# Kernel tuning notes

Measured on AMD Instinct MI355X. Metric: run time of the kernel, lower is better.

## Reference

```python
import jax, jax.numpy as jnp
import numpy as np

# dims
Z, P, N, H = 16, 4, 466, 86          # z_dim, p_dim, n_dim, gmean(466,16)
B_SZ, T = 2048, 32                   # batch, number of eval times
INNER = 16                           # fixed trial-step budget per eval interval
ATOL, RTOL = 1e-20, 1e-5
H2B, H3B = 64, 2048                  # B-net hiddens: int(sqrt(16**3)), 16**3//2

# Dormand-Prince 5(4) tableau
A21 = 1/5
A31, A32 = 3/40, 9/40
A41, A42, A43 = 44/45, -56/15, 32/9
A51, A52, A53, A54 = 19372/6561, -25360/2187, 64448/6561, -212/729
A61, A62, A63, A64, A65 = 9017/3168, -355/33, 46732/5247, 49/176, -5103/18656
B1, B3, B4, B5, B6 = 35/384, 500/1113, 125/192, -2187/6784, 11/84
E1, E3, E4, E5, E6, E7 = 71/57600, -71/16695, 71/1920, -17253/339200, 22/525, -1/40


def _leaky(x):
    return jnp.where(x >= 0, x, 0.2 * x)


def setup_inputs() -> dict:
    key = jax.random.key(0)
    ks = jax.random.split(key, 26)
    w = lambda k, shape: (jax.random.normal(k, shape) * 0.05).astype(jnp.float32)
    inp = {}
    inp['n_0'] = jax.random.normal(ks[0], (B_SZ, N), dtype=jnp.float32)
    inp['p'] = jax.random.uniform(ks[1], (P,), dtype=jnp.float32)
    inp['tstep'] = jnp.arange(T, dtype=jnp.float32) / (T - 1)
    # autoencoder
    inp['We1'], inp['be1'] = w(ks[2], (N, H)), w(ks[3], (H,))
    inp['We2'], inp['be2'] = w(ks[4], (H, Z)), w(ks[5], (Z,))
    inp['Wd1'], inp['bd1'] = w(ks[6], (Z, H)), w(ks[7], (H,))
    inp['Wd2'], inp['bd2'] = w(ks[8], (H, N)), w(ks[9], (N,))
    # A net: P -> Z -> Z*Z//2 -> Z*Z
    inp['Wa1'], inp['ba1'] = w(ks[10], (P, Z)), w(ks[11], (Z,))
    inp['Wa2'], inp['ba2'] = w(ks[12], (Z, Z*Z//2)), w(ks[13], (Z*Z//2,))
    inp['Wa3'], inp['ba3'] = w(ks[14], (Z*Z//2, Z*Z)), w(ks[15], (Z*Z,))
    # B net: P -> Z -> 64 -> 2048 -> Z**3
    inp['Wb1'], inp['bb1'] = w(ks[16], (P, Z)), w(ks[17], (Z,))
    inp['Wb2'], inp['bb2'] = w(ks[18], (Z, H2B)), w(ks[19], (H2B,))
    inp['Wb3'], inp['bb3'] = w(ks[20], (H2B, H3B)), w(ks[21], (H3B,))
    inp['Wb4'], inp['bb4'] = w(ks[22], (H3B, Z**3)), w(ks[23], (Z**3,))
    return inp


def _solve(z0, tstep, Amat, Bten):
    # adaptive Dopri5 with integral (I) step-size controller; fixed trial budget per interval
    def f(z):  # g(z,p): A z + B z z
        return z @ Amat.T + jnp.einsum('ijk,bj,bk->bi', Bten, z, z)

    def step(y, dt):
        k1 = f(y)
        k2 = f(y + dt * (A21 * k1))
        k3 = f(y + dt * (A31 * k1 + A32 * k2))
        k4 = f(y + dt * (A41 * k1 + A42 * k2 + A43 * k3))
        k5 = f(y + dt * (A51 * k1 + A52 * k2 + A53 * k3 + A54 * k4))
        k6 = f(y + dt * (A61 * k1 + A62 * k2 + A63 * k3 + A64 * k4 + A65 * k5))
        y5 = y + dt * (B1 * k1 + B3 * k3 + B4 * k4 + B5 * k5 + B6 * k6)
        k7 = f(y5)
        err = dt * (E1 * k1 + E3 * k3 + E4 * k4 + E5 * k5 + E6 * k6 + E7 * k7)
        return y5, err

    def interval(carry, tpair):
        y, dt = carry
        t0, t1 = tpair[0], tpair[1]

        def inner(c, _):
            t, y, dt = c
            done = t >= t1 - 1e-10
            dtc = jnp.where(done, 0.0, jnp.minimum(dt, t1 - t))  # clip to interval end
            ynew, err = step(y, dtc)
            tol = ATOL + RTOL * jnp.maximum(jnp.abs(y), jnp.abs(ynew))
            en = jnp.sqrt(jnp.mean((err / tol) ** 2))
            accept = (en <= 1.0) & (~done)
            t = jnp.where(accept, t + dtc, t)
            y = jnp.where(accept, ynew, y)
            factor = jnp.clip(0.9 * jnp.maximum(en, 1e-12) ** -0.2, 0.2, 10.0)
            dt = jnp.where(done, dt, dt * factor)
            return (t, y, dt), None

        (tf, yf, dtf), _ = jax.lax.scan(inner, (t0, y, dt), None, length=INNER)
        return (yf, dtf), yf

    dt0 = (tstep[1] - tstep[0]) * 0.3
    tpairs = jnp.stack([tstep[:-1], tstep[1:]], axis=1)  # [T-1, 2]
    (_, _), ys = jax.lax.scan(interval, (z0, dt0), tpairs)
    return jnp.concatenate([z0[None], ys], axis=0)  # [T, b, Z]


def reference(n_0, p, tstep, We1, be1, We2, be2, Wd1, bd1, Wd2, bd2,
              Wa1, ba1, Wa2, ba2, Wa3, ba3,
              Wb1, bb1, Wb2, bb2, Wb3, bb3, Wb4, bb4):
    # encoder
    z0 = _leaky(n_0 @ We1 + be1) @ We2 + be2  # [b, Z]
    # A(p), B(p) depend only on p -> computed once per solve
    ha = _leaky(p @ Wa1 + ba1)
    ha = _leaky(ha @ Wa2 + ba2)
    Amat = _leaky(ha @ Wa3 + ba3).reshape(Z, Z)
    hb = _leaky(p @ Wb1 + bb1)
    hb = _leaky(hb @ Wb2 + bb2)
    hb = _leaky(hb @ Wb3 + bb3)
    Bten = _leaky(hb @ Wb4 + bb4).reshape(Z, Z, Z)
    zs = _solve(z0, tstep, Amat, Bten)  # [T, b, Z]
    # decoder
    return _leaky(zs @ Wd1 + bd1) @ Wd2 + bd2  # [T, b, N]
```

## Files before the change

### kernel.cpp

```cpp
#include <hip/hip_runtime.h>
#include <cmath>

#define DEV __device__ __forceinline__

static DEV float leakyf(float x){ return x >= 0.0f ? x : 0.2f*x; }

typedef float v2f __attribute__((ext_vector_type(2)));

constexpr float cA21 = (float)(1.0/5.0);
constexpr float cA31 = (float)(3.0/40.0),  cA32 = (float)(9.0/40.0);
constexpr float cA41 = (float)(44.0/45.0), cA42 = (float)(-56.0/15.0), cA43 = (float)(32.0/9.0);
constexpr float cA51 = (float)(19372.0/6561.0), cA52 = (float)(-25360.0/2187.0);
constexpr float cA53 = (float)(64448.0/6561.0), cA54 = (float)(-212.0/729.0);
constexpr float cA61 = (float)(9017.0/3168.0),  cA62 = (float)(-355.0/33.0);
constexpr float cA63 = (float)(46732.0/5247.0), cA64 = (float)(49.0/176.0);
constexpr float cA65 = (float)(-5103.0/18656.0);
constexpr float cB1 = (float)(35.0/384.0),  cB3 = (float)(500.0/1113.0), cB4 = (float)(125.0/192.0);
constexpr float cB5 = (float)(-2187.0/6784.0), cB6 = (float)(11.0/84.0);
constexpr float cE1 = (float)(71.0/57600.0), cE3 = (float)(-71.0/16695.0), cE4 = (float)(71.0/1920.0);
constexpr float cE5 = (float)(-17253.0/339200.0), cE6 = (float)(22.0/525.0), cE7 = (float)(-1.0/40.0);

#define WS_AMAT   0
#define WS_HB3    256
#define WS_BTEN   2304
#define WS_ZS     6400
#define WS_SLOTSF (6400 + 1048576)
#define WS_SB2    (WS_SLOTSF + 253952)

__global__ void __launch_bounds__(256) k_smallnets(
    const float* __restrict__ p,
    const float* __restrict__ Wa1, const float* __restrict__ ba1,
    const float* __restrict__ Wa2, const float* __restrict__ ba2,
    const float* __restrict__ Wa3, const float* __restrict__ ba3,
    const float* __restrict__ Wb1, const float* __restrict__ bb1,
    const float* __restrict__ Wb2, const float* __restrict__ bb2,
    float* __restrict__ wsf)
{
    __shared__ float sp[4], sa1[16], sa2[128], sb1[16];
    int tid = threadIdx.x;
    if (tid < 4) sp[tid] = p[tid];
    __syncthreads();
    if (tid < 16) {
        float a = ba1[tid];
        for (int j = 0; j < 4; ++j) a = fmaf(sp[j], Wa1[j*16+tid], a);
        sa1[tid] = leakyf(a);
        float c = bb1[tid];
        for (int j = 0; j < 4; ++j) c = fmaf(sp[j], Wb1[j*16+tid], c);
        sb1[tid] = leakyf(c);
    }
    __syncthreads();
    if (tid < 128) {
        float a = ba2[tid];
        for (int j = 0; j < 16; ++j) a = fmaf(sa1[j], Wa2[j*128+tid], a);
        sa2[tid] = leakyf(a);
    }
    if (tid < 64) {
        float c = bb2[tid];
        for (int j = 0; j < 16; ++j) c = fmaf(sb1[j], Wb2[j*64+tid], c);
        wsf[WS_SB2 + tid] = leakyf(c);
    }
    __syncthreads();
    {
        float a = ba3[tid];
        for (int j = 0; j < 128; ++j) a = fmaf(sa2[j], Wa3[j*256+tid], a);
        wsf[WS_AMAT + tid] = leakyf(a);
    }
}

__global__ void __launch_bounds__(256) k_hb3(
    const float* __restrict__ Wb3, const float* __restrict__ bb3, float* __restrict__ wsf)
{
    __shared__ float sb2[64];
    int tid = threadIdx.x;
    if (tid < 64) sb2[tid] = wsf[WS_SB2 + tid];
    __syncthreads();
    int o = blockIdx.x * 256 + tid;
    float c = bb3[o];
    for (int j = 0; j < 64; ++j) c = fmaf(sb2[j], Wb3[(size_t)j*2048 + o], c);
    wsf[WS_HB3 + o] = leakyf(c);
}

__global__ void __launch_bounds__(256) k_bten(
    const float* __restrict__ Wb4, const float* __restrict__ bb4, float* __restrict__ wsf)
{
    __shared__ float red[256];
    const float* hb3 = wsf + WS_HB3;
    float* Bten = wsf + WS_BTEN;
    int tid = threadIdx.x;
    int ol = tid & 15, part = tid >> 4;
    int o = blockIdx.x * 16 + ol;
    float a = 0.0f;
    for (int q = 0; q < 128; ++q) {
        int hh = part*128 + q;
        a = fmaf(hb3[hh], Wb4[(size_t)hh*4096 + o], a);
    }
    red[part*16 + ol] = a;
    __syncthreads();
    for (int s = 8; s >= 1; s >>= 1) {
        if (part < s) red[part*16+ol] += red[(part+s)*16+ol];
        __syncthreads();
    }
    if (tid < 16) {
        float v = red[tid] + bb4[blockIdx.x*16 + tid];
        Bten[blockIdx.x*16 + tid] = leakyf(v);
    }
}

__global__ void __launch_bounds__(256) k_encoder(
    const float* __restrict__ n0,
    const float* __restrict__ We1, const float* __restrict__ be1,
    const float* __restrict__ We2, const float* __restrict__ be2,
    float* __restrict__ zs)
{
    __shared__ float hL[8][88];
    int tid = threadIdx.x;
    int r = tid >> 5, c = tid & 31;
    int row = blockIdx.x * 8 + r;
    const float* nrow = n0 + (size_t)row * 466;
    int c2 = (c + 64 < 86) ? (c + 64) : 85;
    float a0 = 0.f, a1 = 0.f, a2 = 0.f;
    for (int n = 0; n < 466; ++n) {
        float nv = nrow[n];
        a0 = fmaf(nv, We1[n*86 + c], a0);
        a1 = fmaf(nv, We1[n*86 + c + 32], a1);
        a2 = fmaf(nv, We1[n*86 + c2], a2);
    }
    hL[r][c]      = leakyf(a0 + be1[c]);
    hL[r][c + 32] = leakyf(a1 + be1[c + 32]);
    if (c < 22) hL[r][c + 64] = leakyf(a2 + be1[c + 64]);
    __syncthreads();
    if (tid < 128) {
        int r2 = tid >> 4, ii = tid & 15;
        int row2 = blockIdx.x * 8 + r2;
        float a = be2[ii];
        #pragma unroll
        for (int hh = 0; hh < 86; ++hh) a = fmaf(hL[r2][hh], We2[hh*16 + ii], a);
        zs[(size_t)row2 * 16 + ii] = a;
    }
}

__global__ void __launch_bounds__(256) k_solver(
    const float* __restrict__ tstep, float* __restrict__ wsf)
{
    __shared__ float zL[8][16];
    __shared__ float redA[2][4], redB[2][4];
    float* Amat = wsf + WS_AMAT;
    float* Bten = wsf + WS_BTEN;
    float* zs   = wsf + WS_ZS;
    unsigned long long* slots = (unsigned long long*)(wsf + WS_SLOTSF);

    const int tid = threadIdx.x, blk = blockIdx.x;
    const int e = tid >> 5, g = tid & 31;
    const int i = g >> 1, h = g & 1, h8 = h * 8;
    const int b = blk * 8 + e;

    v2f Bl2[64], aR2[8];
    #pragma unroll
    for (int p = 0; p < 8; ++p) {
        int jA = (h8 + 2*p)     & 15;
        int jB = (h8 + 2*p + 1) & 15;
        v2f ap; ap.x = (h == 0) ? Amat[i*16 + 2*p] : 0.0f;
        ap.y = (h == 0) ? Amat[i*16 + 2*p + 1] : 0.0f;
        aR2[p] = ap;
        const float4* bpA = (const float4*)(Bten + i*256 + jA*16 + h8);
        const float4* bpB = (const float4*)(Bten + i*256 + jB*16 + h8);
        float4 a0 = bpA[0], a1 = bpA[1], b0 = bpB[0], b1 = bpB[1];
        v2f q;
        q.x=a0.x; q.y=b0.x; Bl2[p*8+0]=q;  q.x=a0.y; q.y=b0.y; Bl2[p*8+1]=q;
        q.x=a0.z; q.y=b0.z; Bl2[p*8+2]=q;  q.x=a0.w; q.y=b0.w; Bl2[p*8+3]=q;
        q.x=a1.x; q.y=b1.x; Bl2[p*8+4]=q;  q.x=a1.y; q.y=b1.y; Bl2[p*8+5]=q;
        q.x=a1.z; q.y=b1.z; Bl2[p*8+6]=q;  q.x=a1.w; q.y=b1.w; Bl2[p*8+7]=q;
    }

    float y = zs[(size_t)b*16 + i];

    auto feval = [&](float zi) -> float {
        zL[e][i] = zi;
        const float4* zp = (const float4*)(&zL[e][0]);
        int q0 = h8 >> 2;
        float4 r0 = zp[q0], r1 = zp[(q0+1)&3], r2 = zp[(q0+2)&3], r3 = zp[(q0+3)&3];
        float zz[16] = { r0.x,r0.y,r0.z,r0.w, r1.x,r1.y,r1.z,r1.w,
                         r2.x,r2.y,r2.z,r2.w, r3.x,r3.y,r3.z,r3.w };
        v2f zb[8];
        #pragma unroll
        for (int kk = 0; kk < 8; ++kk) { v2f t; t.x = zz[kk]; t.y = zz[kk]; zb[kk] = t; }
        v2f t2[8];
        #pragma unroll
        for (int p = 0; p < 8; ++p) t2[p] = aR2[p];
        #pragma unroll
        for (int p = 0; p < 8; ++p) {
            #pragma unroll
            for (int kk = 0; kk < 8; ++kk)
                asm("v_pk_fma_f32 %0, %1, %2, %0" : "+v"(t2[p]) : "v"(Bl2[p*8+kk]), "v"(zb[kk]));
        }
        float acc = 0.0f;
        #pragma unroll
        for (int p = 0; p < 8; ++p) {
            acc = fmaf(zz[2*p],     t2[p].x, acc);
            acc = fmaf(zz[2*p + 1], t2[p].y, acc);
        }
        acc += __shfl_xor(acc, 1);
        return acc;
    };

    float dt = (tstep[1] - tstep[0]) * 0.3f;
    float k1 = feval(y), k2, k3, k4, k5, k6, k7;
    int stepIdx = 0;

    for (int iv = 0; iv < 31; ++iv) {
        float t  = tstep[iv];
        float t1 = tstep[iv + 1];
        for (int it = 0; it < 16; ++it) {
            if (t >= t1 - 1e-10f) break;
            float dtc = fminf(dt, t1 - t);

            float z2 = fmaf(dtc, cA21*k1, y);                                         k2 = feval(z2);
            float z3 = fmaf(dtc, fmaf(cA32,k2, cA31*k1), y);                          k3 = feval(z3);
            float z4 = fmaf(dtc, fmaf(cA43,k3, fmaf(cA42,k2, cA41*k1)), y);           k4 = feval(z4);
            float z5 = fmaf(dtc, fmaf(cA54,k4, fmaf(cA53,k3, fmaf(cA52,k2, cA51*k1))), y);
            k5 = feval(z5);
            float z6 = fmaf(dtc, fmaf(cA65,k5, fmaf(cA64,k4, fmaf(cA63,k3, fmaf(cA62,k2, cA61*k1)))), y);
            k6 = feval(z6);
            float y5 = fmaf(dtc, fmaf(cB6,k6, fmaf(cB5,k5, fmaf(cB4,k4, fmaf(cB3,k3, cB1*k1)))), y);
            k7 = feval(y5);
            float err = dtc * fmaf(cE7,k7, fmaf(cE6,k6, fmaf(cE5,k5, fmaf(cE4,k4, fmaf(cE3,k3, cE1*k1)))));

            float ay = fabsf(y), a5 = fabsf(y5);
            float mx = (ay > a5) ? ay : a5;
            float tol = fmaf(1e-5f, mx, 1e-20f);
            float r = err / tol;
            float r2 = r * r;

            const int par = stepIdx & 1;

            float w = r2;
            w += __shfl_xor(w, 1);  w += __shfl_xor(w, 2);  w += __shfl_xor(w, 4);
            w += __shfl_xor(w, 8);  w += __shfl_xor(w, 16); w += __shfl_xor(w, 32);
            if ((tid & 63) == 0) redA[par][tid >> 6] = w;
            __syncthreads();
            float bsum = ((redA[par][0] + redA[par][1]) + redA[par][2]) + redA[par][3];

            unsigned long long* rowp = slots + (size_t)stepIdx * 256;
            if (tid == 0) {
                unsigned long long pv = (1ull << 32) | (unsigned long long)__float_as_uint(bsum);
                __hip_atomic_store(&rowp[blk], pv, __ATOMIC_RELAXED, __HIP_MEMORY_SCOPE_AGENT);
            }
            unsigned long long v = __hip_atomic_load(&rowp[tid], __ATOMIC_RELAXED, __HIP_MEMORY_SCOPE_AGENT);
            if ((unsigned)(v >> 32) != 1u) {
                for (;;) {
                    unsigned long long va = __hip_atomic_load(&rowp[tid], __ATOMIC_RELAXED, __HIP_MEMORY_SCOPE_AGENT);
                    unsigned long long vb = __hip_atomic_load(&rowp[tid], __ATOMIC_RELAXED, __HIP_MEMORY_SCOPE_AGENT);
                    if ((unsigned)(va >> 32) == 1u) { v = va; break; }
                    if ((unsigned)(vb >> 32) == 1u) { v = vb; break; }
                }
            }
            float ps = __uint_as_float((unsigned)v);
            ps += __shfl_xor(ps, 1);  ps += __shfl_xor(ps, 2);  ps += __shfl_xor(ps, 4);
            ps += __shfl_xor(ps, 8);  ps += __shfl_xor(ps, 16); ps += __shfl_xor(ps, 32);
            if ((tid & 63) == 0) redB[par][tid >> 6] = ps;
            __syncthreads();
            float gsum = ((redB[par][0] + redB[par][1]) + redB[par][2]) + redB[par][3];
            ++stepIdx;

            float en = sqrtf(gsum * (1.0f / 65536.0f));

            if (!(en == en)) {
                if (h == 0) {
                    for (int s = iv + 1; s < 32; ++s)
                        zs[((size_t)s * 2048 + b) * 16 + i] = y;
                }
                return;
            }
            if (en <= 1.0f) { t = t + dtc; y = y5; k1 = k7; }
            float fac = 0.9f * powf(fmaxf(en, 1e-12f), -0.2f);
            fac = fminf(fmaxf(fac, 0.2f), 10.0f);
            dt = dt * fac;
        }
        if (h == 0) zs[((size_t)(iv + 1) * 2048 + b) * 16 + i] = y;
    }
}

__global__ void __launch_bounds__(256) k_decoder(
    const float* __restrict__ zs,
    const float* __restrict__ Wd1, const float* __restrict__ bd1,
    const float* __restrict__ Wd2, const float* __restrict__ bd2,
    float* __restrict__ out)
{
    __shared__ __align__(16) float hT[86][16];
    int tid = threadIdx.x;
    size_t rowbase = (size_t)blockIdx.x * 16;

    for (int v = tid; v < 86*16; v += 256) {
        int hh = v >> 4, r = v & 15;
        const float4* z4 = (const float4*)(zs + (rowbase + r) * 16);
        float4 za = z4[0], zb = z4[1], zc = z4[2], zd = z4[3];
        float a = bd1[hh];
        a = fmaf(za.x, Wd1[ 0*86 + hh], a);  a = fmaf(za.y, Wd1[ 1*86 + hh], a);
        a = fmaf(za.z, Wd1[ 2*86 + hh], a);  a = fmaf(za.w, Wd1[ 3*86 + hh], a);
        a = fmaf(zb.x, Wd1[ 4*86 + hh], a);  a = fmaf(zb.y, Wd1[ 5*86 + hh], a);
        a = fmaf(zb.z, Wd1[ 6*86 + hh], a);  a = fmaf(zb.w, Wd1[ 7*86 + hh], a);
        a = fmaf(zc.x, Wd1[ 8*86 + hh], a);  a = fmaf(zc.y, Wd1[ 9*86 + hh], a);
        a = fmaf(zc.z, Wd1[10*86 + hh], a);  a = fmaf(zc.w, Wd1[11*86 + hh], a);
        a = fmaf(zd.x, Wd1[12*86 + hh], a);  a = fmaf(zd.y, Wd1[13*86 + hh], a);
        a = fmaf(zd.z, Wd1[14*86 + hh], a);  a = fmaf(zd.w, Wd1[15*86 + hh], a);
        hT[hh][r] = leakyf(a);
    }
    __syncthreads();

    for (int c = tid; c < 466; c += 256) {
        float acc[16];
        #pragma unroll
        for (int r = 0; r < 16; ++r) acc[r] = bd2[c];
        for (int hh = 0; hh < 86; ++hh) {
            float w = Wd2[hh*466 + c];
            const float4* hp = (const float4*)(&hT[hh][0]);
            float4 h0 = hp[0], h1 = hp[1], h2 = hp[2], h3 = hp[3];
            acc[ 0] = fmaf(h0.x, w, acc[ 0]);  acc[ 1] = fmaf(h0.y, w, acc[ 1]);
            acc[ 2] = fmaf(h0.z, w, acc[ 2]);  acc[ 3] = fmaf(h0.w, w, acc[ 3]);
            acc[ 4] = fmaf(h1.x, w, acc[ 4]);  acc[ 5] = fmaf(h1.y, w, acc[ 5]);
            acc[ 6] = fmaf(h1.z, w, acc[ 6]);  acc[ 7] = fmaf(h1.w, w, acc[ 7]);
            acc[ 8] = fmaf(h2.x, w, acc[ 8]);  acc[ 9] = fmaf(h2.y, w, acc[ 9]);
            acc[10] = fmaf(h2.z, w, acc[10]);  acc[11] = fmaf(h2.w, w, acc[11]);
            acc[12] = fmaf(h3.x, w, acc[12]);  acc[13] = fmaf(h3.y, w, acc[13]);
            acc[14] = fmaf(h3.z, w, acc[14]);  acc[15] = fmaf(h3.w, w, acc[15]);
        }
        #pragma unroll
        for (int r = 0; r < 16; ++r) out[(rowbase + r) * 466 + c] = acc[r];
    }
}

extern "C" void kernel_launch(void* const* d_in, const int* in_sizes, int n_in,
                              void* d_out, int out_size, void* d_ws, size_t ws_size,
                              hipStream_t stream)
{
    const float* n0   = (const float*)d_in[0];
    const float* p    = (const float*)d_in[1];
    const float* tstep= (const float*)d_in[2];
    const float* We1  = (const float*)d_in[3];  const float* be1 = (const float*)d_in[4];
    const float* We2  = (const float*)d_in[5];  const float* be2 = (const float*)d_in[6];
    const float* Wd1  = (const float*)d_in[7];  const float* bd1 = (const float*)d_in[8];
    const float* Wd2  = (const float*)d_in[9];  const float* bd2 = (const float*)d_in[10];
    const float* Wa1  = (const float*)d_in[11]; const float* ba1 = (const float*)d_in[12];
    const float* Wa2  = (const float*)d_in[13]; const float* ba2 = (const float*)d_in[14];
    const float* Wa3  = (const float*)d_in[15]; const float* ba3 = (const float*)d_in[16];
    const float* Wb1  = (const float*)d_in[17]; const float* bb1 = (const float*)d_in[18];
    const float* Wb2  = (const float*)d_in[19]; const float* bb2 = (const float*)d_in[20];
    const float* Wb3  = (const float*)d_in[21]; const float* bb3 = (const float*)d_in[22];
    const float* Wb4  = (const float*)d_in[23]; const float* bb4 = (const float*)d_in[24];
    float* out = (float*)d_out;
    float* wsf = (float*)d_ws;

    hipLaunchKernelGGL(k_smallnets, dim3(1), dim3(256), 0, stream,
                       p, Wa1, ba1, Wa2, ba2, Wa3, ba3, Wb1, bb1, Wb2, bb2, wsf);
    hipLaunchKernelGGL(k_hb3, dim3(8), dim3(256), 0, stream, Wb3, bb3, wsf);
    hipLaunchKernelGGL(k_bten, dim3(256), dim3(256), 0, stream, Wb4, bb4, wsf);
    hipLaunchKernelGGL(k_encoder, dim3(256), dim3(256), 0, stream,
                       n0, We1, be1, We2, be2, wsf + WS_ZS);

    hipLaunchKernelGGL(k_solver, dim3(256), dim3(256), 0, stream, tstep, wsf);

    hipLaunchKernelGGL(k_decoder, dim3(4096), dim3(256), 0, stream,
                       wsf + WS_ZS, Wd1, bd1, Wd2, bd2, out);
}
```

Before: 1.349 ms.

## Fuse encoder into solver kernel and exchange state via ds_bpermute

Moves the encoder computation into the start of the solver kernel, so z0 is produced in shared memory and one kernel launch plus the global round-trip are removed. It also replaces the per-stage shared-memory write and float4 reads of the state vector inside feval with 16 ds_bpermute cross-lane reads, which removes LDS stores and the associated synchronisation-like dependency. The trade-off is more register pressure for the permutation indices and 16 bpermute instructions per evaluation instead of four vector LDS loads.

```diff
diff --git a/kernel.cpp b/kernel.cpp
--- a/kernel.cpp
+++ b/kernel.cpp
@@ -106,43 +106,15 @@
     }
 }
 
-__global__ void __launch_bounds__(256) k_encoder(
+__global__ void __launch_bounds__(256) k_solver(
+    const float* __restrict__ tstep,
     const float* __restrict__ n0,
     const float* __restrict__ We1, const float* __restrict__ be1,
     const float* __restrict__ We2, const float* __restrict__ be2,
-    float* __restrict__ zs)
-{
-    __shared__ float hL[8][88];
-    int tid = threadIdx.x;
-    int r = tid >> 5, c = tid & 31;
-    int row = blockIdx.x * 8 + r;
-    const float* nrow = n0 + (size_t)row * 466;
-    int c2 = (c + 64 < 86) ? (c + 64) : 85;
-    float a0 = 0.f, a1 = 0.f, a2 = 0.f;
-    for (int n = 0; n < 466; ++n) {
-        float nv = nrow[n];
-        a0 = fmaf(nv, We1[n*86 + c], a0);
-        a1 = fmaf(nv, We1[n*86 + c + 32], a1);
-        a2 = fmaf(nv, We1[n*86 + c2], a2);
-    }
-    hL[r][c]      = leakyf(a0 + be1[c]);
-    hL[r][c + 32] = leakyf(a1 + be1[c + 32]);
-    if (c < 22) hL[r][c + 64] = leakyf(a2 + be1[c + 64]);
-    __syncthreads();
-    if (tid < 128) {
-        int r2 = tid >> 4, ii = tid & 15;
-        int row2 = blockIdx.x * 8 + r2;
-        float a = be2[ii];
-        #pragma unroll
-        for (int hh = 0; hh < 86; ++hh) a = fmaf(hL[r2][hh], We2[hh*16 + ii], a);
-        zs[(size_t)row2 * 16 + ii] = a;
-    }
-}
-
-__global__ void __launch_bounds__(256) k_solver(
-    const float* __restrict__ tstep, float* __restrict__ wsf)
-{
-    __shared__ float zL[8][16];
+    float* __restrict__ wsf)
+{
+    __shared__ float hE[8][88];
+    __shared__ float zE[8][16];
     __shared__ float redA[2][4], redB[2][4];
     float* Amat = wsf + WS_AMAT;
     float* Bten = wsf + WS_BTEN;
@@ -153,6 +125,33 @@
     const int e = tid >> 5, g = tid & 31;
     const int i = g >> 1, h = g & 1, h8 = h * 8;
     const int b = blk * 8 + e;
+
+    {
+        int r = tid >> 5, c = tid & 31;
+        int row = blk * 8 + r;
+        const float* nrow = n0 + (size_t)row * 466;
+        int c2 = (c + 64 < 86) ? (c + 64) : 85;
+        float a0 = 0.f, a1 = 0.f, a2 = 0.f;
+        for (int n = 0; n < 466; ++n) {
+            float nv = nrow[n];
+            a0 = fmaf(nv, We1[n*86 + c], a0);
+            a1 = fmaf(nv, We1[n*86 + c + 32], a1);
+            a2 = fmaf(nv, We1[n*86 + c2], a2);
+        }
+        hE[r][c]      = leakyf(a0 + be1[c]);
+        hE[r][c + 32] = leakyf(a1 + be1[c + 32]);
+        if (c < 22) hE[r][c + 64] = leakyf(a2 + be1[c + 64]);
+        __syncthreads();
+        if (tid < 128) {
+            int r2 = tid >> 4, ii = tid & 15;
+            float a = be2[ii];
+            #pragma unroll
+            for (int hh = 0; hh < 86; ++hh) a = fmaf(hE[r2][hh], We2[hh*16 + ii], a);
+            zE[r2][ii] = a;
+            zs[((size_t)(blk*8 + r2)) * 16 + ii] = a;
+        }
+        __syncthreads();
+    }
 
     v2f Bl2[64], aR2[8];
     #pragma unroll
@@ -172,15 +171,19 @@
         q.x=a1.z; q.y=b1.z; Bl2[p*8+6]=q;  q.x=a1.w; q.y=b1.w; Bl2[p*8+7]=q;
     }
 
-    float y = zs[(size_t)b*16 + i];
+    int prm[16];
+    #pragma unroll
+    for (int m = 0; m < 16; ++m)
+        prm[m] = ((tid & 32) + (((h8 + m) & 15) << 1)) << 2;
+
+    float y = zE[e][i];
 
     auto feval = [&](float zi) -> float {
-        zL[e][i] = zi;
-        const float4* zp = (const float4*)(&zL[e][0]);
-        int q0 = h8 >> 2;
-        float4 r0 = zp[q0], r1 = zp[(q0+1)&3], r2 = zp[(q0+2)&3], r3 = zp[(q0+3)&3];
-        float zz[16] = { r0.x,r0.y,r0.z,r0.w, r1.x,r1.y,r1.z,r1.w,
-                         r2.x,r2.y,r2.z,r2.w, r3.x,r3.y,r3.z,r3.w };
+        int zib = __float_as_int(zi);
+        float zz[16];
+        #pragma unroll
+        for (int m = 0; m < 16; ++m)
+            zz[m] = __int_as_float(__builtin_amdgcn_ds_bpermute(prm[m], zib));
         v2f zb[8];
         #pragma unroll
         for (int kk = 0; kk < 8; ++kk) { v2f t; t.x = zz[kk]; t.y = zz[kk]; zb[kk] = t; }
@@ -354,10 +357,9 @@
                        p, Wa1, ba1, Wa2, ba2, Wa3, ba3, Wb1, bb1, Wb2, bb2, wsf);
     hipLaunchKernelGGL(k_hb3, dim3(8), dim3(256), 0, stream, Wb3, bb3, wsf);
     hipLaunchKernelGGL(k_bten, dim3(256), dim3(256), 0, stream, Wb4, bb4, wsf);
-    hipLaunchKernelGGL(k_encoder, dim3(256), dim3(256), 0, stream,
-                       n0, We1, be1, We2, be2, wsf + WS_ZS);
-
-    hipLaunchKernelGGL(k_solver, dim3(256), dim3(256), 0, stream, tstep, wsf);
+
+    hipLaunchKernelGGL(k_solver, dim3(256), dim3(256), 0, stream,
+                       tstep, n0, We1, be1, We2, be2, wsf);
 
     hipLaunchKernelGGL(k_decoder, dim3(4096), dim3(256), 0, stream,
                        wsf + WS_ZS, Wd1, bd1, Wd2, bd2, out);
```

After: 1.439 ms. 1.07x slower.
